# Kernel optimization log

Hardware: AMD Instinct MI355X
Metric: run time of the kernel (lower is better)

The kernel has to match this reference:

```python
import jax, jax.numpy as jnp
import numpy as np

H = 16  # n_heads
MAX_LEN = 1024


def _skew(x):
    # x: (B, H, N, M) with M == N. Pad 1 column on the left, reshape, drop first row.
    B, h, N, M = x.shape
    x = jnp.pad(x, ((0, 0), (0, 0), (0, 0), (1, 0)))  # (B,H,N,M+1)
    x = x.reshape(B, h, M + 1, N)
    return x[:, :, 1:, :]  # (B,H,N,N)


def setup_inputs() -> dict:
    key = jax.random.key(0)
    ks = jax.random.split(key, 10)
    B, N, C, T = 8, 1024, 1024, 256
    s = 0.02
    return {
        "x": jax.random.normal(ks[0], (B, N, C), dtype=jnp.float32),
        "time_emb": jax.random.normal(ks[1], (B, T), dtype=jnp.float32),
        "W_qkv": jax.random.normal(ks[2], (C, 3 * C), dtype=jnp.float32) * s,
        "b_qkv": jnp.zeros((3 * C,), dtype=jnp.float32),
        "W_time": jax.random.normal(ks[3], (T, 3 * C), dtype=jnp.float32) * s,
        "b_time": jnp.zeros((3 * C,), dtype=jnp.float32),
        "W_out": jax.random.normal(ks[4], (C, C), dtype=jnp.float32) * s,
        "b_out": jnp.zeros((C,), dtype=jnp.float32),
        "Er": jax.random.normal(ks[5], (MAX_LEN, C // H), dtype=jnp.float32) * s,
    }


def reference(x, time_emb, W_qkv, b_qkv, W_time, b_time, W_out, b_out, Er):
    B, N, C = x.shape
    D = C // H
    # token qkv: (B,N,3C) -> (3,B,H,N,D)
    qkv = (x @ W_qkv + b_qkv).reshape(B, N, 3, H, D).transpose(2, 0, 3, 1, 4)
    q, k, v = qkv[0], qkv[1], qkv[2]
    # time qkv: (B,3C) -> (3,B,H,1,D)
    tqkv = (time_emb @ W_time + b_time).reshape(B, 1, 3, H, D).transpose(2, 0, 3, 1, 4)
    q = q + tqkv[0]
    k = k + tqkv[1]
    v = v + tqkv[2]
    # relative position bias
    Er_sl = Er[Er.shape[0] - N:]                      # (N, D)
    rel = jnp.einsum('bhnd,md->bhnm', q, Er_sl)        # (B,H,N,N)
    rel = _skew(rel)
    scale = D ** (-0.5)
    scores = jnp.einsum('bhnd,bhmd->bhnm', q, k) * scale + rel
    attn = jax.nn.softmax(scores, axis=-1)
    out = jnp.einsum('bhnm,bhmd->bhnd', attn, v)       # (B,H,N,D)
    out = out.transpose(0, 2, 1, 3).reshape(B, N, C)
    return out @ W_out + b_out
```

## Files before the change

### kernel.cpp

```cpp
#include <hip/hip_runtime.h>
#include <math.h>

typedef __attribute__((ext_vector_type(8))) short short8;
typedef __attribute__((ext_vector_type(8))) unsigned short ushort8;
typedef __attribute__((ext_vector_type(4))) unsigned short us4;
typedef __attribute__((ext_vector_type(4))) float f32x4;

#define NH 16
#define HD 64
#define SEQ 1024
#define NB 8
#define CH 1024
#define TD 256
#define GROW 1025
#define LOG2E 1.4426950408889634f

__device__ __forceinline__ unsigned short f2bf(float f) {
  union { float f; unsigned int u; } v; v.f = f;
  unsigned int r = v.u + 0x7FFFu + ((v.u >> 16) & 1u);
  return (unsigned short)(r >> 16);
}
__device__ __forceinline__ float bf2f(unsigned short s) {
  union { unsigned int u; float f; } v; v.u = ((unsigned int)s) << 16;
  return v.f;
}
__device__ __forceinline__ float hexp2(float x) {
  float r;
  asm("v_exp_f32 %0, %1" : "=v"(r) : "v"(x));
  return r;
}
__device__ __forceinline__ void gload_lds16(const unsigned short* g, unsigned short* l) {
  __builtin_amdgcn_global_load_lds(
      (const __attribute__((address_space(1))) unsigned int*)g,
      (__attribute__((address_space(3))) unsigned int*)l, 16, 0, 0);
}

__global__ __launch_bounds__(256) void time_proj_kernel(
    const float* __restrict__ time_emb, const float* __restrict__ W_time,
    const float* __restrict__ b_time, float* __restrict__ tqkv) {
  int idx = blockIdx.x * 256 + threadIdx.x;
  if (idx >= NB * 3072) return;
  int b = idx / 3072, c = idx % 3072;
  float s = b_time[c];
  for (int t = 0; t < TD; ++t) s += time_emb[b * TD + t] * W_time[t * 3072 + c];
  tqkv[idx] = s;
}

__global__ __launch_bounds__(256) void er_convert_kernel(
    const float* __restrict__ Er, unsigned short* __restrict__ Er_bf) {
  int i = blockIdx.x * 256 + threadIdx.x;
  if (i < SEQ * HD) Er_bf[i] = f2bf(Er[i] * LOG2E);
}

__global__ __launch_bounds__(256) void convert_bf_kernel(
    const float* __restrict__ in, unsigned short* __restrict__ out, int n8) {
  int i = blockIdx.x * 256 + threadIdx.x;
  if (i >= n8) return;
  float4 a = ((const float4*)in)[2 * i];
  float4 b = ((const float4*)in)[2 * i + 1];
  ushort8 o;
  o[0] = f2bf(a.x); o[1] = f2bf(a.y); o[2] = f2bf(a.z); o[3] = f2bf(a.w);
  o[4] = f2bf(b.x); o[5] = f2bf(b.y); o[6] = f2bf(b.z); o[7] = f2bf(b.w);
  ((ushort8*)out)[i] = o;
}

__global__ __launch_bounds__(256) void transpose_bf_kernel(
    const float* __restrict__ W, unsigned short* __restrict__ Wt, int R, int Cc) {
  __shared__ float T[64][65];
  int r0 = blockIdx.y * 64, c0 = blockIdx.x * 64;
  for (int idx = threadIdx.x; idx < 4096; idx += 256) {
    int r = idx >> 6, c = idx & 63;
    T[r][c] = W[(size_t)(r0 + r) * Cc + c0 + c];
  }
  __syncthreads();
  for (int idx = threadIdx.x; idx < 4096; idx += 256) {
    int c = idx >> 6, r = idx & 63;
    Wt[(size_t)(c0 + c) * R + r0 + r] = f2bf(T[r][c]);
  }
}

__global__ __launch_bounds__(256) void qkv_gemm_mfma(
    const unsigned short* __restrict__ A, const unsigned short* __restrict__ Bt,
    const float* __restrict__ bqkv, const float* __restrict__ tqkv,
    unsigned short* __restrict__ qb, unsigned short* __restrict__ ksw,
    unsigned short* __restrict__ vtsw) {
  __shared__ unsigned short As[128 * 32];
  __shared__ unsigned short Bs[128 * 32];
  const int m0 = blockIdx.x * 128, n0 = blockIdx.y * 128;
  const int tid = threadIdx.x, l = tid & 63, w = tid >> 6;
  const int wm = w >> 1, wn = w & 1;
  const int grp = l >> 4, col = l & 15;
  f32x4 acc[4][4];
#pragma unroll
  for (int mi = 0; mi < 4; ++mi)
#pragma unroll
    for (int ni = 0; ni < 4; ++ni) acc[mi][ni] = (f32x4){0.f, 0.f, 0.f, 0.f};

  for (int k0 = 0; k0 < 1024; k0 += 32) {
    __syncthreads();
#pragma unroll
    for (int i = 0; i < 2; ++i) {
      int seg = i * 256 + w * 64 + l;
      int mr = seg >> 2, kq = seg & 3;
      gload_lds16(A + (size_t)(m0 + mr) * 1024 + k0 + kq * 8,
                  &As[(i * 256 + w * 64) * 8]);
      gload_lds16(Bt + (size_t)(n0 + mr) * 1024 + k0 + kq * 8,
                  &Bs[(i * 256 + w * 64) * 8]);
    }
    __syncthreads();
    short8 af[4], bfv[4];
#pragma unroll
    for (int mi = 0; mi < 4; ++mi)
      af[mi] = *(const short8*)&As[(wm * 64 + mi * 16 + col) * 32 + grp * 8];
#pragma unroll
    for (int ni = 0; ni < 4; ++ni)
      bfv[ni] = *(const short8*)&Bs[(wn * 64 + ni * 16 + col) * 32 + grp * 8];
#pragma unroll
    for (int mi = 0; mi < 4; ++mi)
#pragma unroll
      for (int ni = 0; ni < 4; ++ni)
        acc[mi][ni] = __builtin_amdgcn_mfma_f32_16x16x32_bf16(af[mi], bfv[ni], acc[mi][ni], 0, 0, 0);
  }

  const int bidx = m0 >> 10;
  const int which = n0 >> 10;
  float biasv[4];
  int hhv[4], dv[4];
#pragma unroll
  for (int ni = 0; ni < 4; ++ni) {
    int c = n0 + wn * 64 + ni * 16 + col;
    biasv[ni] = bqkv[c] + tqkv[bidx * 3072 + c];
    int cc = c & 1023;
    hhv[ni] = cc >> 6;
    dv[ni] = cc & 63;
  }
  if (which == 2) {
    int t = (m0 & 1023) + wm * 64;
#pragma unroll
    for (int ni = 0; ni < 4; ++ni) {
      size_t rowb = ((size_t)(bidx * 16 + hhv[ni]) * 64 + dv[ni]) * 1024;
      int swz = (dv[ni] & 7) << 3;
#pragma unroll
      for (int rr = 0; rr < 4; ++rr) {
        int kbase = (grp * 4 + rr) * 4;
        int colix = t + ((kbase & ~7) ^ swz) + (kbase & 7);
        us4 pk;
#pragma unroll
        for (int mi = 0; mi < 4; ++mi) pk[mi] = f2bf(acc[mi][ni][rr] + biasv[ni]);
        *(us4*)&vtsw[rowb + colix] = pk;
      }
    }
  } else if (which == 1) {
#pragma unroll
    for (int mi = 0; mi < 4; ++mi)
#pragma unroll
      for (int rr = 0; rr < 4; ++rr) {
        int nn = (m0 + wm * 64 + mi * 16 + grp * 4 + rr) & 1023;
#pragma unroll
        for (int ni = 0; ni < 4; ++ni) {
          size_t bhh = (size_t)(bidx * 16 + hhv[ni]);
          ksw[(bhh * 1024 + nn) * 64 + (dv[ni] ^ ((nn & 7) << 3))] =
              f2bf(acc[mi][ni][rr] + biasv[ni]);
        }
      }
  } else {
#pragma unroll
    for (int mi = 0; mi < 4; ++mi)
#pragma unroll
      for (int rr = 0; rr < 4; ++rr) {
        int nn = (m0 + wm * 64 + mi * 16 + grp * 4 + rr) & 1023;
#pragma unroll
        for (int ni = 0; ni < 4; ++ni) {
          size_t bhh = (size_t)(bidx * 16 + hhv[ni]);
          qb[(bhh * 1024 + nn) * 64 + dv[ni]] = f2bf(acc[mi][ni][rr] + biasv[ni]);
        }
      }
  }
}

__global__ __launch_bounds__(256) void out_gemm_mfma(
    const unsigned short* __restrict__ A, const unsigned short* __restrict__ Bt,
    const float* __restrict__ bias, float* __restrict__ out) {
  __shared__ unsigned short As[128 * 32];
  __shared__ unsigned short Bs[128 * 32];
  const int m0 = blockIdx.x * 128, n0 = blockIdx.y * 128;
  const int tid = threadIdx.x, l = tid & 63, w = tid >> 6;
  const int wm = w >> 1, wn = w & 1;
  const int grp = l >> 4, col = l & 15;
  f32x4 acc[4][4];
#pragma unroll
  for (int mi = 0; mi < 4; ++mi)
#pragma unroll
    for (int ni = 0; ni < 4; ++ni) acc[mi][ni] = (f32x4){0.f, 0.f, 0.f, 0.f};

  for (int k0 = 0; k0 < 1024; k0 += 32) {
    __syncthreads();
#pragma unroll
    for (int i = 0; i < 2; ++i) {
      int seg = i * 256 + w * 64 + l;
      int mr = seg >> 2, kq = seg & 3;
      gload_lds16(A + (size_t)(m0 + mr) * 1024 + k0 + kq * 8,
                  &As[(i * 256 + w * 64) * 8]);
      gload_lds16(Bt + (size_t)(n0 + mr) * 1024 + k0 + kq * 8,
                  &Bs[(i * 256 + w * 64) * 8]);
    }
    __syncthreads();
    short8 af[4], bfv[4];
#pragma unroll
    for (int mi = 0; mi < 4; ++mi)
      af[mi] = *(const short8*)&As[(wm * 64 + mi * 16 + col) * 32 + grp * 8];
#pragma unroll
    for (int ni = 0; ni < 4; ++ni)
      bfv[ni] = *(const short8*)&Bs[(wn * 64 + ni * 16 + col) * 32 + grp * 8];
#pragma unroll
    for (int mi = 0; mi < 4; ++mi)
#pragma unroll
      for (int ni = 0; ni < 4; ++ni)
        acc[mi][ni] = __builtin_amdgcn_mfma_f32_16x16x32_bf16(af[mi], bfv[ni], acc[mi][ni], 0, 0, 0);
  }
  float bv[4];
#pragma unroll
  for (int ni = 0; ni < 4; ++ni) bv[ni] = bias[n0 + wn * 64 + ni * 16 + col];
#pragma unroll
  for (int mi = 0; mi < 4; ++mi)
#pragma unroll
    for (int rr = 0; rr < 4; ++rr) {
      int row = m0 + wm * 64 + mi * 16 + grp * 4 + rr;
#pragma unroll
      for (int ni = 0; ni < 4; ++ni) {
        int c = n0 + wn * 64 + ni * 16 + col;
        out[(size_t)row * 1024 + c] = acc[mi][ni][rr] + bv[ni];
      }
    }
}

__global__ __launch_bounds__(256) void g_gemm2(
    const unsigned short* __restrict__ qb, int bh_base,
    const unsigned short* __restrict__ Er_bf,
    unsigned short* __restrict__ Gp) {
  const int n0 = blockIdx.x * 64;
  const int jq = blockIdx.y;
  const int bhl = blockIdx.z;
  const int bh = bh_base + bhl;
  const int tid = threadIdx.x, l = tid & 63, w = tid >> 6;
  const int grp = l >> 4, col = l & 15;
  const int jw = jq * 256 + w * 64;

  short8 aq[4][2];
#pragma unroll
  for (int rf = 0; rf < 4; ++rf)
#pragma unroll
    for (int dc = 0; dc < 2; ++dc)
      aq[rf][dc] = *(const short8*)(qb + ((size_t)bh * SEQ + n0 + rf * 16 + col) * HD + dc * 32 + grp * 8);

  f32x4 acc[4][4];
#pragma unroll
  for (int rf = 0; rf < 4; ++rf)
#pragma unroll
    for (int cf = 0; cf < 4; ++cf) acc[rf][cf] = (f32x4){0.f, 0.f, 0.f, 0.f};

#pragma unroll
  for (int cf = 0; cf < 4; ++cf)
#pragma unroll
    for (int dc = 0; dc < 2; ++dc) {
      short8 bfrag = *(const short8*)(Er_bf + (size_t)(jw + cf * 16 + col) * HD + dc * 32 + grp * 8);
#pragma unroll
      for (int rf = 0; rf < 4; ++rf)
        acc[rf][cf] = __builtin_amdgcn_mfma_f32_16x16x32_bf16(aq[rf][dc], bfrag, acc[rf][cf], 0, 0, 0);
    }

#pragma unroll
  for (int rf = 0; rf < 4; ++rf)
#pragma unroll
    for (int cf = 0; cf < 4; ++cf)
#pragma unroll
      for (int rr = 0; rr < 4; ++rr) {
        int n = n0 + rf * 16 + grp * 4 + rr;
        int j = jw + cf * 16 + col;
        Gp[((size_t)(bhl * SEQ + n)) * GROW + j] = f2bf(acc[rf][cf][rr]);
      }
  if (jq == 3 && tid < 64) {
    int n = n0 + tid;
    Gp[((size_t)(bhl * SEQ + n)) * GROW + 1024] = 0;
  }
}

__global__ __launch_bounds__(256) void attn_kernel(
    const unsigned short* __restrict__ qb, const unsigned short* __restrict__ ksw,
    const unsigned short* __restrict__ vtsw, const unsigned short* __restrict__ Gp,
    unsigned short* __restrict__ attn_o, int bh_base) {
  __shared__ __align__(16) unsigned short KsL[2][4096];
  __shared__ __align__(16) unsigned short VtL[2][4096];
  __shared__ __align__(16) unsigned short Band[2][64][72];
  __shared__ __align__(16) unsigned short Pw[4][16][72];

  const int wg = blockIdx.x + 16 * blockIdx.y;
  const int chunk = 2 * gridDim.y;
  const int nid = (wg & 7) * chunk + (wg >> 3);
  const int bhl = nid >> 4;
  const int n0 = (nid & 15) * 64;
  const int bh = bh_base + bhl;
  const int b = bh >> 4, h = bh & 15;
  const int tid = threadIdx.x, lane = tid & 63, wq = tid >> 6;
  const int grp = lane >> 4, col = lane & 15;
  const int n0w = n0 + wq * 16;

  short8 aq[2];
#pragma unroll
  for (int dc = 0; dc < 2; ++dc)
    aq[dc] = *(const short8*)(qb + ((size_t)(bh * SEQ + n0w + col)) * HD + dc * 32 + grp * 8);

  f32x4 acco[4];
#pragma unroll
  for (int oc = 0; oc < 4; ++oc) acco[oc] = (f32x4){0.f, 0.f, 0.f, 0.f};
  float mrun[4], lrun[4];
#pragma unroll
  for (int r = 0; r < 4; ++r) { mrun[r] = -INFINITY; lrun[r] = 0.f; }

  const float scale2 = 0.125f * LOG2E;
  const unsigned short* kbh = ksw + (size_t)bh * SEQ * HD;
  const unsigned short* vbh = vtsw + (size_t)bh * HD * SEQ;
  const unsigned short* gbase = Gp + (size_t)(bhl * SEQ + n0) * GROW + (1016 - n0);

  auto STAGE = [&](int buf, int m0) {
#pragma unroll
    for (int i = 0; i < 2; ++i) {
      int gi = i * 256 + wq * 64 + lane;
      int row = gi >> 3, gc = gi & 7;
      gload_lds16(kbh + (((size_t)(m0 + row)) << 6) + gc * 8,
                  &KsL[buf][(i * 256 + wq * 64) * 8]);
      gload_lds16(vbh + (((size_t)row) << 10) + m0 + gc * 8,
                  &VtL[buf][(i * 256 + wq * 64) * 8]);
    }
    const unsigned short* gsrc = gbase + m0;
    unsigned short* bdst = &Band[buf][0][0];
    const int g0 = wq * 144;
#pragma unroll
    for (int it = 0; it < 2; ++it) {
      int g = g0 + it * 64 + lane;
      int r = g / 9, seg = g - r * 9;
      gload_lds16(gsrc + r * 1024 + seg * 8, bdst + g * 8);
    }
    if (lane < 16) {
      int g = g0 + 128 + lane;
      int r = g / 9, seg = g - r * 9;
      gload_lds16(gsrc + r * 1024 + seg * 8, bdst + g * 8);
    }
  };

  STAGE(0, 0);
  __syncthreads();

  for (int t = 0; t < 16; ++t) {
    const int cur = t & 1;
    if (t < 15) STAGE(cur ^ 1, (t + 1) * 64);
    f32x4 acc[4];
#pragma unroll
    for (int mc = 0; mc < 4; ++mc) acc[mc] = (f32x4){0.f, 0.f, 0.f, 0.f};
#pragma unroll
    for (int mc = 0; mc < 4; ++mc)
#pragma unroll
      for (int dc = 0; dc < 2; ++dc) {
        short8 bk = *(const short8*)&KsL[cur][(mc * 16 + col) * 64 + (((dc * 4 + grp) ^ (col & 7)) << 3)];
        acc[mc] = __builtin_amdgcn_mfma_f32_16x16x32_bf16(aq[dc], bk, acc[mc], 0, 0, 0);
      }
#pragma unroll
    for (int r = 0; r < 4; ++r) {
      int dr = wq * 16 + grp * 4 + r;
      float s[4];
#pragma unroll
      for (int mc = 0; mc < 4; ++mc)
        s[mc] = fmaf(acc[mc][r], scale2, bf2f(Band[cur][dr][7 + mc * 16 + col]));
      float mx = fmaxf(fmaxf(s[0], s[1]), fmaxf(s[2], s[3]));
#pragma unroll
      for (int off = 1; off < 16; off <<= 1) mx = fmaxf(mx, __shfl_xor(mx, off));
      if (mx > mrun[r]) {
        float cr = hexp2(mrun[r] - mx);
        mrun[r] = mx;
        lrun[r] *= cr;
#pragma unroll
        for (int oc = 0; oc < 4; ++oc) acco[oc][r] *= cr;
      }
      float p0 = hexp2(s[0] - mrun[r]);
      float p1 = hexp2(s[1] - mrun[r]);
      float p2 = hexp2(s[2] - mrun[r]);
      float p3 = hexp2(s[3] - mrun[r]);
      lrun[r] += (p0 + p1) + (p2 + p3);
      unsigned int r01, r23;
      asm("v_cvt_pk_bf16_f32 %0, %1, %2" : "=v"(r01) : "v"(p0), "v"(p1));
      asm("v_cvt_pk_bf16_f32 %0, %1, %2" : "=v"(r23) : "v"(p2), "v"(p3));
      unsigned long long pk = (unsigned long long)r01 | ((unsigned long long)r23 << 32);
      *(unsigned long long*)&Pw[wq][grp * 4 + r][col * 4] = pk;
    }
    short8 ap[2];
#pragma unroll
    for (int kc = 0; kc < 2; ++kc)
      ap[kc] = *(const short8*)&Pw[wq][col][kc * 32 + grp * 8];
#pragma unroll
    for (int oc = 0; oc < 4; ++oc)
#pragma unroll
      for (int kc = 0; kc < 2; ++kc) {
        short8 bv = *(const short8*)&VtL[cur][(oc * 16 + col) * 64 + (((kc * 4 + grp) ^ (col & 7)) << 3)];
        acco[oc] = __builtin_amdgcn_mfma_f32_16x16x32_bf16(ap[kc], bv, acco[oc], 0, 0, 0);
      }
    __syncthreads();
  }
#pragma unroll
  for (int r = 0; r < 4; ++r) {
    float tot = lrun[r];
#pragma unroll
    for (int off = 1; off < 16; off <<= 1) tot += __shfl_xor(tot, off);
    float inv = 1.0f / tot;
    int n = n0w + grp * 4 + r;
#pragma unroll
    for (int oc = 0; oc < 4; ++oc) {
      int d = oc * 16 + col;
      attn_o[((size_t)(b * SEQ + n)) * CH + h * HD + d] = f2bf(acco[oc][r] * inv);
    }
  }
}

extern "C" void kernel_launch(void* const* d_in, const int* in_sizes, int n_in,
                              void* d_out, int out_size, void* d_ws, size_t ws_size,
                              hipStream_t stream) {
  const float* x        = (const float*)d_in[0];
  const float* time_emb = (const float*)d_in[1];
  const float* W_qkv    = (const float*)d_in[2];
  const float* b_qkv    = (const float*)d_in[3];
  const float* W_time   = (const float*)d_in[4];
  const float* b_time   = (const float*)d_in[5];
  const float* W_out    = (const float*)d_in[6];
  const float* b_out    = (const float*)d_in[7];
  const float* Er       = (const float*)d_in[8];
  float* out = (float*)d_out;

  char* p = (char*)d_ws;
  float* tqkv = (float*)p;                      p += 98304;
  unsigned short* qb = (unsigned short*)p;      p += 16777216;
  unsigned short* ksw = (unsigned short*)p;     p += 16777216;
  unsigned short* vtsw = (unsigned short*)p;    p += 16777216;
  unsigned short* attn_o = (unsigned short*)p;  p += 16777216;
  unsigned short* Er_bf = (unsigned short*)p;   p += 131072;
  unsigned short* Wout_t = (unsigned short*)p;  p += 2097152;
  unsigned short* x_bf = (unsigned short*)p;
  unsigned short* Wqkv_t = x_bf + (size_t)8388608;
  unsigned short* Gp = (unsigned short*)p;

  size_t fixed = (size_t)(p - (char*)d_ws);
  int slab_bh = (ws_size >= fixed + (size_t)64 * 2099200) ? 64 : 32;
  int nslab = 128 / slab_bh;

  er_convert_kernel<<<256, 256, 0, stream>>>(Er, Er_bf);
  time_proj_kernel<<<96, 256, 0, stream>>>(time_emb, W_time, b_time, tqkv);
  convert_bf_kernel<<<4096, 256, 0, stream>>>(x, x_bf, 1048576);
  transpose_bf_kernel<<<dim3(48, 16), 256, 0, stream>>>(W_qkv, Wqkv_t, 1024, 3072);
  transpose_bf_kernel<<<dim3(16, 16), 256, 0, stream>>>(W_out, Wout_t, 1024, 1024);
  qkv_gemm_mfma<<<dim3(64, 24), 256, 0, stream>>>(x_bf, Wqkv_t, b_qkv, tqkv, qb, ksw, vtsw);
  for (int s = 0; s < nslab; ++s) {
    int bh_base = s * slab_bh;
    g_gemm2<<<dim3(16, 4, slab_bh), 256, 0, stream>>>(qb, bh_base, Er_bf, Gp);
    attn_kernel<<<dim3(16, slab_bh), 256, 0, stream>>>(qb, ksw, vtsw, Gp, attn_o, bh_base);
  }
  out_gemm_mfma<<<dim3(64, 8), 256, 0, stream>>>(attn_o, Wout_t, b_out, out);
}
```

Baseline: 383.7 us.

## Transpose attention MFMA operands so each lane owns one query row

The QK^T and PV MFMAs now take their operands in swapped order, so the accumulator is transposed and each lane holds a single query row with 16 key columns. The online softmax then needs only one running max and one running sum per lane, with two cross-lane shuffles instead of four per row, and P and the output are written with wider vector stores. The change also wraps the MFMA blocks in s_setprio and adds an occupancy hint to the QKV GEMM launch bounds. The aim is to cut shuffle and VALU overhead in the softmax, in exchange for a different LDS access pattern on the band and P buffers.

```diff
diff --git a/kernel.cpp b/kernel.cpp
--- a/kernel.cpp
+++ b/kernel.cpp
@@ -4,6 +4,7 @@
 typedef __attribute__((ext_vector_type(8))) short short8;
 typedef __attribute__((ext_vector_type(8))) unsigned short ushort8;
 typedef __attribute__((ext_vector_type(4))) unsigned short us4;
+typedef __attribute__((ext_vector_type(4))) unsigned int u32x4;
 typedef __attribute__((ext_vector_type(4))) float f32x4;
 
 #define NH 16
@@ -79,7 +80,7 @@
   }
 }
 
-__global__ __launch_bounds__(256) void qkv_gemm_mfma(
+__global__ __launch_bounds__(256, 6) void qkv_gemm_mfma(
     const unsigned short* __restrict__ A, const unsigned short* __restrict__ Bt,
     const float* __restrict__ bqkv, const float* __restrict__ tqkv,
     unsigned short* __restrict__ qb, unsigned short* __restrict__ ksw,
@@ -313,9 +314,7 @@
   f32x4 acco[4];
 #pragma unroll
   for (int oc = 0; oc < 4; ++oc) acco[oc] = (f32x4){0.f, 0.f, 0.f, 0.f};
-  float mrun[4], lrun[4];
-#pragma unroll
-  for (int r = 0; r < 4; ++r) { mrun[r] = -INFINITY; lrun[r] = 0.f; }
+  float mrun = -INFINITY, lrun = 0.f;
 
   const float scale2 = 0.125f * LOG2E;
   const unsigned short* kbh = ksw + (size_t)bh * SEQ * HD;
@@ -357,66 +356,81 @@
     f32x4 acc[4];
 #pragma unroll
     for (int mc = 0; mc < 4; ++mc) acc[mc] = (f32x4){0.f, 0.f, 0.f, 0.f};
+    __builtin_amdgcn_s_setprio(1);
 #pragma unroll
     for (int mc = 0; mc < 4; ++mc)
 #pragma unroll
       for (int dc = 0; dc < 2; ++dc) {
         short8 bk = *(const short8*)&KsL[cur][(mc * 16 + col) * 64 + (((dc * 4 + grp) ^ (col & 7)) << 3)];
-        acc[mc] = __builtin_amdgcn_mfma_f32_16x16x32_bf16(aq[dc], bk, acc[mc], 0, 0, 0);
-      }
-#pragma unroll
-    for (int r = 0; r < 4; ++r) {
-      int dr = wq * 16 + grp * 4 + r;
-      float s[4];
-#pragma unroll
-      for (int mc = 0; mc < 4; ++mc)
-        s[mc] = fmaf(acc[mc][r], scale2, bf2f(Band[cur][dr][7 + mc * 16 + col]));
-      float mx = fmaxf(fmaxf(s[0], s[1]), fmaxf(s[2], s[3]));
-#pragma unroll
-      for (int off = 1; off < 16; off <<= 1) mx = fmaxf(mx, __shfl_xor(mx, off));
-      if (mx > mrun[r]) {
-        float cr = hexp2(mrun[r] - mx);
-        mrun[r] = mx;
-        lrun[r] *= cr;
-#pragma unroll
-        for (int oc = 0; oc < 4; ++oc) acco[oc][r] *= cr;
-      }
-      float p0 = hexp2(s[0] - mrun[r]);
-      float p1 = hexp2(s[1] - mrun[r]);
-      float p2 = hexp2(s[2] - mrun[r]);
-      float p3 = hexp2(s[3] - mrun[r]);
-      lrun[r] += (p0 + p1) + (p2 + p3);
-      unsigned int r01, r23;
-      asm("v_cvt_pk_bf16_f32 %0, %1, %2" : "=v"(r01) : "v"(p0), "v"(p1));
-      asm("v_cvt_pk_bf16_f32 %0, %1, %2" : "=v"(r23) : "v"(p2), "v"(p3));
-      unsigned long long pk = (unsigned long long)r01 | ((unsigned long long)r23 << 32);
-      *(unsigned long long*)&Pw[wq][grp * 4 + r][col * 4] = pk;
-    }
+        acc[mc] = __builtin_amdgcn_mfma_f32_16x16x32_bf16(bk, aq[dc], acc[mc], 0, 0, 0);
+      }
+    __builtin_amdgcn_s_setprio(0);
+    float s[4][4];
+    const int dr = wq * 16 + col;
+#pragma unroll
+    for (int mc = 0; mc < 4; ++mc)
+#pragma unroll
+      for (int r = 0; r < 4; ++r)
+        s[mc][r] = fmaf(acc[mc][r], scale2, bf2f(Band[cur][dr][7 + mc * 16 + grp * 4 + r]));
+    float mx = s[0][0];
+#pragma unroll
+    for (int mc = 0; mc < 4; ++mc)
+#pragma unroll
+      for (int r = 0; r < 4; ++r) mx = fmaxf(mx, s[mc][r]);
+    mx = fmaxf(mx, __shfl_xor(mx, 16));
+    mx = fmaxf(mx, __shfl_xor(mx, 32));
+    if (mx > mrun) {
+      float cr = hexp2(mrun - mx);
+      mrun = mx;
+      lrun *= cr;
+#pragma unroll
+      for (int oc = 0; oc < 4; ++oc)
+#pragma unroll
+        for (int r = 0; r < 4; ++r) acco[oc][r] *= cr;
+    }
+    float p[4][4];
+#pragma unroll
+    for (int mc = 0; mc < 4; ++mc)
+#pragma unroll
+      for (int r = 0; r < 4; ++r) {
+        p[mc][r] = hexp2(s[mc][r] - mrun);
+        lrun += p[mc][r];
+      }
+    unsigned int wpk[8];
+#pragma unroll
+    for (int r = 0; r < 4; ++r)
+#pragma unroll
+      for (int mh = 0; mh < 2; ++mh)
+        asm("v_cvt_pk_bf16_f32 %0, %1, %2"
+            : "=v"(wpk[r * 2 + mh]) : "v"(p[mh * 2][r]), "v"(p[mh * 2 + 1][r]));
+    *(u32x4*)&Pw[wq][col][grp * 16] = (u32x4){wpk[0], wpk[1], wpk[2], wpk[3]};
+    *(u32x4*)&Pw[wq][col][grp * 16 + 8] = (u32x4){wpk[4], wpk[5], wpk[6], wpk[7]};
     short8 ap[2];
 #pragma unroll
     for (int kc = 0; kc < 2; ++kc)
       ap[kc] = *(const short8*)&Pw[wq][col][kc * 32 + grp * 8];
+    __builtin_amdgcn_s_setprio(1);
 #pragma unroll
     for (int oc = 0; oc < 4; ++oc)
 #pragma unroll
       for (int kc = 0; kc < 2; ++kc) {
         short8 bv = *(const short8*)&VtL[cur][(oc * 16 + col) * 64 + (((kc * 4 + grp) ^ (col & 7)) << 3)];
-        acco[oc] = __builtin_amdgcn_mfma_f32_16x16x32_bf16(ap[kc], bv, acco[oc], 0, 0, 0);
-      }
+        acco[oc] = __builtin_amdgcn_mfma_f32_16x16x32_bf16(bv, ap[kc], acco[oc], 0, 0, 0);
+      }
+    __builtin_amdgcn_s_setprio(0);
     __syncthreads();
   }
-#pragma unroll
-  for (int r = 0; r < 4; ++r) {
-    float tot = lrun[r];
-#pragma unroll
-    for (int off = 1; off < 16; off <<= 1) tot += __shfl_xor(tot, off);
-    float inv = 1.0f / tot;
-    int n = n0w + grp * 4 + r;
-#pragma unroll
-    for (int oc = 0; oc < 4; ++oc) {
-      int d = oc * 16 + col;
-      attn_o[((size_t)(b * SEQ + n)) * CH + h * HD + d] = f2bf(acco[oc][r] * inv);
-    }
+  float tot = lrun;
+  tot += __shfl_xor(tot, 16);
+  tot += __shfl_xor(tot, 32);
+  float inv = 1.0f / tot;
+  const int n = n0w + col;
+#pragma unroll
+  for (int oc = 0; oc < 4; ++oc) {
+    us4 pk;
+#pragma unroll
+    for (int r = 0; r < 4; ++r) pk[r] = f2bf(acco[oc][r] * inv);
+    *(us4*)&attn_o[((size_t)(b * SEQ + n)) * CH + h * HD + oc * 16 + grp * 4] = pk;
   }
 }
 
```

Result: slower. 811.0 us (+111.3%).
